# Optimization experiments

Measured on AMD Instinct MI355X. Metric: run time of the kernel, lower is better.

## Reference

```python
import jax, jax.numpy as jnp
import numpy as np

V, H, O = 32, 256, 256  # input_dim, hidden_dim, output_dim
EPS = 1e-5


def _layer_norm(x, g, b):
    m = jnp.mean(x, axis=-1, keepdims=True)
    v = jnp.mean((x - m) ** 2, axis=-1, keepdims=True)
    return g * (x - m) * jax.lax.rsqrt(v + EPS) + b


def setup_inputs() -> dict:
    key = jax.random.key(0)
    ks = jax.random.split(key, 20)
    s = 0.05
    inp = {
        "x": jax.random.normal(ks[0], (16, 256, V), dtype=jnp.float32),
        # selection GRN (input_dim -> input_dim, identity skip)
        "sel_fc1_w": jax.random.normal(ks[1], (V, H), dtype=jnp.float32) * s,
        "sel_fc1_b": jnp.zeros((H,), jnp.float32),
        "sel_fc2_w": jax.random.normal(ks[2], (H, V), dtype=jnp.float32) * s,
        "sel_fc2_b": jnp.zeros((V,), jnp.float32),
        "sel_gate_w": jax.random.normal(ks[3], (V, 2 * V), dtype=jnp.float32) * s,
        "sel_gate_b": jnp.zeros((2 * V,), jnp.float32),
        "sel_ln_g": jnp.ones((V,), jnp.float32),
        "sel_ln_b": jnp.zeros((V,), jnp.float32),
        # per-variable GRNs, stacked over the V variables (each has in_dim=1)
        "var_fc1_w": jax.random.normal(ks[4], (V, H), dtype=jnp.float32) * s,
        "var_fc1_b": jnp.zeros((V, H), jnp.float32),
        "var_fc2_w": jax.random.normal(ks[5], (V, H, O), dtype=jnp.float32) * s,
        "var_fc2_b": jnp.zeros((V, O), jnp.float32),
        "var_gate_w": jax.random.normal(ks[6], (V, 2 * O), dtype=jnp.float32) * s,
        "var_gate_b": jnp.zeros((V, 2 * O), jnp.float32),
        "var_skip_w": jax.random.normal(ks[7], (V, O), dtype=jnp.float32) * s,
        "var_skip_b": jnp.zeros((V, O), jnp.float32),
        "var_ln_g": jnp.ones((V, O), jnp.float32),
        "var_ln_b": jnp.zeros((V, O), jnp.float32),
    }
    return inp


def _vsn_forward(x, sel_fc1_w, sel_fc1_b, sel_fc2_w, sel_fc2_b, sel_gate_w,
                 sel_gate_b, sel_ln_g, sel_ln_b, var_fc1_w, var_fc1_b,
                 var_fc2_w, var_fc2_b, var_gate_w, var_gate_b, var_skip_w,
                 var_skip_b, var_ln_g, var_ln_b):
    B, S, _ = x.shape
    xr = x.reshape(-1, V)  # [N, V]

    # --- selection GRN (skip is identity) ---
    h = jax.nn.elu(xr @ sel_fc1_w + sel_fc1_b)        # [N, H]
    h = h @ sel_fc2_w + sel_fc2_b                      # [N, V] (unused by residual; matches torch code)
    g = xr @ sel_gate_w + sel_gate_b                   # [N, 2V]
    gates, values = jnp.split(g, 2, axis=-1)
    glu = jax.nn.sigmoid(gates) * values               # [N, V]
    sel = _layer_norm(glu + xr, sel_ln_g, sel_ln_b)    # [N, V]
    weights = jax.nn.softmax(sel, axis=-1)             # [N, V]

    # --- batched per-variable GRNs (in_dim = 1) ---
    xv = xr[..., None]                                  # [N, V, 1]
    hv = jax.nn.elu(xv * var_fc1_w + var_fc1_b)         # [N, V, H]
    hv = jnp.einsum('nvh,vho->nvo', hv, var_fc2_w) + var_fc2_b  # [N, V, O]
    gv = xv * var_gate_w + var_gate_b                   # [N, V, 2O]
    gates_v, values_v = jnp.split(gv, 2, axis=-1)
    glu_v = jax.nn.sigmoid(gates_v) * values_v          # [N, V, O]
    skip_v = xv * var_skip_w + var_skip_b               # [N, V, O]
    proc = _layer_norm(glu_v + skip_v, var_ln_g, var_ln_b)  # [N, V, O]

    out = jnp.einsum('nv,nvo->no', weights, proc)       # [N, O]
    return out.reshape(B, S, O)


def reference(x, sel_fc1_w, sel_fc1_b, sel_fc2_w, sel_fc2_b, sel_gate_w,
              sel_gate_b, sel_ln_g, sel_ln_b, var_fc1_w, var_fc1_b,
              var_fc2_w, var_fc2_b, var_gate_w, var_gate_b, var_skip_w,
              var_skip_b, var_ln_g, var_ln_b):
    return _vsn_forward(x, sel_fc1_w, sel_fc1_b, sel_fc2_w, sel_fc2_b,
                        sel_gate_w, sel_gate_b, sel_ln_g, sel_ln_b,
                        var_fc1_w, var_fc1_b, var_fc2_w, var_fc2_b,
                        var_gate_w, var_gate_b, var_skip_w, var_skip_b,
                        var_ln_g, var_ln_b)
```

## Files before the change

### kernel.cpp

```cpp
#include <hip/hip_runtime.h>
#include <hip/hip_bf16.h>


#define VDIM 32
#define ODIM 256
#define RPB  16
#define TPB  1024
#define NCHUNK  16

__device__ __forceinline__ float fast_sigmoid(float g) {
    return __builtin_amdgcn_rcpf(1.0f + __expf(-g));
}

template <int CTRL>
__device__ __forceinline__ float dpp_add(float x) {
    int s = __builtin_amdgcn_update_dpp(0, __builtin_bit_cast(int, x),
                                        CTRL, 0xF, 0xF, true);
    return x + __builtin_bit_cast(float, s);
}

__device__ __forceinline__ float wave_sum(float x) {
    x = dpp_add<0x111>(x);
    x = dpp_add<0x112>(x);
    x = dpp_add<0x114>(x);
    x = dpp_add<0x118>(x);
    x = dpp_add<0x142>(x);
    x = dpp_add<0x143>(x);
    return __builtin_bit_cast(float,
        __builtin_amdgcn_readlane(__builtin_bit_cast(int, x), 63));
}

__global__ void __launch_bounds__(TPB) vsn_fused(
    const float* __restrict__ x,
    const float* __restrict__ sgw,
    const float* __restrict__ sgb,
    const float* __restrict__ slg,
    const float* __restrict__ slb,
    const float* __restrict__ vgw,
    const float* __restrict__ vgb,
    const float* __restrict__ vsw,
    const float* __restrict__ vsb,
    const float* __restrict__ vlg,
    const float* __restrict__ vlb,
    float* __restrict__ out)
{
    __shared__ float wbuf[2][4096];
    __shared__ float x_s[RPB][VDIM];
    __shared__ float g_s[RPB][2 * VDIM];
    __shared__ float w_s[RPB][VDIM];

    const int tid  = threadIdx.x;
    const int row0 = blockIdx.x * RPB;

    const float* sbase;
    int sstr;
    if (tid < 256)      { sbase = vgw + (tid << 2);         sstr = 1024; }
    else if (tid < 512) { sbase = vgb + ((tid - 256) << 2); sstr = 1024; }
    else if (tid < 640) { sbase = vsw + ((tid - 512) << 2); sstr = 512;  }
    else if (tid < 768) { sbase = vsb + ((tid - 640) << 2); sstr = 512;  }
    else if (tid < 896) { sbase = vlg + ((tid - 768) << 2); sstr = 512;  }
    else                { sbase = vlb + ((tid - 896) << 2); sstr = 512;  }

    const float4 st0 = *(const float4*)sbase;

    if (tid < RPB * VDIM)
        ((float*)x_s)[tid] = x[row0 * VDIM + tid];
    __syncthreads();

    {
        const int r = tid >> 6, j = tid & 63;
        float acc = sgb[j];
        #pragma unroll
        for (int v = 0; v < VDIM; ++v)
            acc = fmaf(x_s[r][v], sgw[v * 64 + j], acc);
        g_s[r][j] = acc;
    }
    __syncthreads();

    ((float4*)wbuf[0])[tid] = st0;

    if (tid < RPB * VDIM) {
        const int r = tid >> 5, v = tid & 31;
        const float gate = g_s[r][v];
        const float val  = g_s[r][VDIM + v];
        const float y    = fast_sigmoid(gate) * val + x_s[r][v];
        float s1 = y, s2 = y * y;
        #pragma unroll
        for (int m = 1; m < 32; m <<= 1) {
            s1 += __shfl_xor(s1, m, 64);
            s2 += __shfl_xor(s2, m, 64);
        }
        const float mean = s1 * (1.0f / VDIM);
        const float var  = s2 * (1.0f / VDIM) - mean * mean;
        const float rs   = __builtin_amdgcn_rsqf(var + 1e-5f);
        const float sel  = slg[v] * ((y - mean) * rs) + slb[v];
        float mx = sel;
        #pragma unroll
        for (int m = 1; m < 32; m <<= 1)
            mx = fmaxf(mx, __shfl_xor(mx, m, 64));
        const float e = __expf(sel - mx);
        float se = e;
        #pragma unroll
        for (int m = 1; m < 32; m <<= 1)
            se += __shfl_xor(se, m, 64);
        w_s[r][v] = e * __builtin_amdgcn_rcpf(se);
    }
    __syncthreads();

    const int wave = tid >> 6;
    const int lane = tid & 63;
    const int o0   = lane << 2;

    float acc0 = 0.0f, acc1 = 0.0f, acc2 = 0.0f, acc3 = 0.0f;

    for (int c = 0; c < NCHUNK; ++c) {
        float4 pf;
        if (c < NCHUNK - 1)
            pf = *(const float4*)(sbase + (c + 1) * sstr);

        const float* buf = wbuf[c & 1];

        #pragma unroll
        for (int v4 = 0; v4 < 2; ++v4) {
            const int v = c * 2 + v4;
            const float4 ga  = *(const float4*)(buf + v4 * 512 + o0);
            const float4 va  = *(const float4*)(buf + v4 * 512 + 256 + o0);
            const float4 gab = *(const float4*)(buf + 1024 + v4 * 512 + o0);
            const float4 vab = *(const float4*)(buf + 1024 + v4 * 512 + 256 + o0);
            const float4 sw4 = *(const float4*)(buf + 2048 + v4 * 256 + o0);
            const float4 sb4 = *(const float4*)(buf + 2560 + v4 * 256 + o0);
            const float4 lg4 = *(const float4*)(buf + 3072 + v4 * 256 + o0);
            const float4 lb4 = *(const float4*)(buf + 3584 + v4 * 256 + o0);

            const float xv = x_s[wave][v];

            const float y0 = fast_sigmoid(fmaf(xv, ga.x, gab.x)) * fmaf(xv, va.x, vab.x) + fmaf(xv, sw4.x, sb4.x);
            const float y1 = fast_sigmoid(fmaf(xv, ga.y, gab.y)) * fmaf(xv, va.y, vab.y) + fmaf(xv, sw4.y, sb4.y);
            const float y2 = fast_sigmoid(fmaf(xv, ga.z, gab.z)) * fmaf(xv, va.z, vab.z) + fmaf(xv, sw4.z, sb4.z);
            const float y3 = fast_sigmoid(fmaf(xv, ga.w, gab.w)) * fmaf(xv, va.w, vab.w) + fmaf(xv, sw4.w, sb4.w);

            const float s1 = wave_sum((y0 + y1) + (y2 + y3));
            const float s2 = wave_sum(fmaf(y0, y0, fmaf(y1, y1, fmaf(y2, y2, y3 * y3))));

            const float mean = s1 * (1.0f / ODIM);
            const float var  = s2 * (1.0f / ODIM) - mean * mean;
            const float rs   = __builtin_amdgcn_rsqf(var + 1e-5f);
            const float wv   = w_s[wave][v];
            const float wrs  = wv * rs;
            acc0 = fmaf(lg4.x, (y0 - mean) * wrs, fmaf(wv, lb4.x, acc0));
            acc1 = fmaf(lg4.y, (y1 - mean) * wrs, fmaf(wv, lb4.y, acc1));
            acc2 = fmaf(lg4.z, (y2 - mean) * wrs, fmaf(wv, lb4.z, acc2));
            acc3 = fmaf(lg4.w, (y3 - mean) * wrs, fmaf(wv, lb4.w, acc3));
        }

        if (c < NCHUNK - 1)
            ((float4*)wbuf[(c + 1) & 1])[tid] = pf;
        __syncthreads();
    }

    float4 o4 = make_float4(acc0, acc1, acc2, acc3);
    *(float4*)(out + (size_t)(row0 + wave) * ODIM + o0) = o4;
}

extern "C" void kernel_launch(void* const* d_in, const int* in_sizes, int n_in,
                              void* d_out, int out_size, void* d_ws, size_t ws_size,
                              hipStream_t stream) {
    const float* x   = (const float*)d_in[0];
    const float* sgw = (const float*)d_in[5];
    const float* sgb = (const float*)d_in[6];
    const float* slg = (const float*)d_in[7];
    const float* slb = (const float*)d_in[8];
    const float* vgw = (const float*)d_in[13];
    const float* vgb = (const float*)d_in[14];
    const float* vsw = (const float*)d_in[15];
    const float* vsb = (const float*)d_in[16];
    const float* vlg = (const float*)d_in[17];
    const float* vlb = (const float*)d_in[18];
    float* out = (float*)d_out;

    const int N = in_sizes[0] / VDIM;
    const int grid = N / RPB;

    vsn_fused<<<grid, TPB, 0, stream>>>(x, sgw, sgb, slg, slb,
                                        vgw, vgb, vsw, vsb, vlg, vlb, out);
}
```

Before: 117.0 us.

## Keep per-variable weights in registers, reduce across waves with LDS atomics

Each wave now owns two variables and keeps their gate, value, skip and layernorm parameters in registers. It loops over all 16 rows of the block, where before each wave owned one row and streamed all the weights through a double-buffered LDS pipeline with a barrier per chunk. Per-row contributions are summed across waves with shared-memory atomicAdd, and the sigmoid folds the -log2(e) scale into the weights so it can use exp2. This removes the 16 barriers and the repeated weight traffic through LDS. In exchange it adds LDS atomic contention, higher register pressure, and a __launch_bounds__ occupancy hint.

```diff
diff --git a/kernel.cpp b/kernel.cpp
--- a/kernel.cpp
+++ b/kernel.cpp
@@ -6,11 +6,6 @@
 #define ODIM 256
 #define RPB  16
 #define TPB  1024
-#define NCHUNK  16
-
-__device__ __forceinline__ float fast_sigmoid(float g) {
-    return __builtin_amdgcn_rcpf(1.0f + __expf(-g));
-}
 
 template <int CTRL>
 __device__ __forceinline__ float dpp_add(float x) {
@@ -30,7 +25,11 @@
         __builtin_amdgcn_readlane(__builtin_bit_cast(int, x), 63));
 }
 
-__global__ void __launch_bounds__(TPB) vsn_fused(
+__device__ __forceinline__ float fast_sigmoid(float g) {
+    return __builtin_amdgcn_rcpf(1.0f + __expf(-g));
+}
+
+__global__ void __launch_bounds__(TPB, 4) vsn_fused(
     const float* __restrict__ x,
     const float* __restrict__ sgw,
     const float* __restrict__ sgb,
@@ -44,24 +43,37 @@
     const float* __restrict__ vlb,
     float* __restrict__ out)
 {
-    __shared__ float wbuf[2][4096];
+    __shared__ float acc_s[RPB * ODIM];
     __shared__ float x_s[RPB][VDIM];
     __shared__ float g_s[RPB][2 * VDIM];
     __shared__ float w_s[RPB][VDIM];
 
     const int tid  = threadIdx.x;
     const int row0 = blockIdx.x * RPB;
+    const int wave = tid >> 6;
+    const int lane = tid & 63;
+    const int v0   = wave * 2;
 
-    const float* sbase;
-    int sstr;
-    if (tid < 256)      { sbase = vgw + (tid << 2);         sstr = 1024; }
-    else if (tid < 512) { sbase = vgb + ((tid - 256) << 2); sstr = 1024; }
-    else if (tid < 640) { sbase = vsw + ((tid - 512) << 2); sstr = 512;  }
-    else if (tid < 768) { sbase = vsb + ((tid - 640) << 2); sstr = 512;  }
-    else if (tid < 896) { sbase = vlg + ((tid - 768) << 2); sstr = 512;  }
-    else                { sbase = vlb + ((tid - 896) << 2); sstr = 512;  }
+    float ga[2][4], gb[2][4], va[2][4], vb[2][4];
+    float sw[2][4], sb[2][4], lg[2][4], lb[2][4];
+    #pragma unroll
+    for (int j = 0; j < 2; ++j) {
+        const int v = v0 + j;
+        #pragma unroll
+        for (int k = 0; k < 4; ++k) {
+            const int c = lane + 64 * k;
+            ga[j][k] = vgw[v * 512 + c];
+            va[j][k] = vgw[v * 512 + 256 + c];
+            gb[j][k] = vgb[v * 512 + c];
+            vb[j][k] = vgb[v * 512 + 256 + c];
+            sw[j][k] = vsw[v * 256 + c];
+            sb[j][k] = vsb[v * 256 + c];
+            lg[j][k] = vlg[v * 256 + c];
+            lb[j][k] = vlb[v * 256 + c];
+        }
+    }
 
-    const float4 st0 = *(const float4*)sbase;
+    *(float4*)(acc_s + (tid << 2)) = make_float4(0.f, 0.f, 0.f, 0.f);
 
     if (tid < RPB * VDIM)
         ((float*)x_s)[tid] = x[row0 * VDIM + tid];
@@ -76,8 +88,6 @@
         g_s[r][j] = acc;
     }
     __syncthreads();
-
-    ((float4*)wbuf[0])[tid] = st0;
 
     if (tid < RPB * VDIM) {
         const int r = tid >> 5, v = tid & 31;
@@ -107,59 +117,57 @@
     }
     __syncthreads();
 
-    const int wave = tid >> 6;
-    const int lane = tid & 63;
-    const int o0   = lane << 2;
+    constexpr float NL2E = -1.4426950408889634f;
+    #pragma unroll
+    for (int j = 0; j < 2; ++j)
+        #pragma unroll
+        for (int k = 0; k < 4; ++k) { ga[j][k] *= NL2E; gb[j][k] *= NL2E; }
 
-    float acc0 = 0.0f, acc1 = 0.0f, acc2 = 0.0f, acc3 = 0.0f;
+    for (int i = 0; i < RPB; ++i) {
+        const int r  = (wave + i) & (RPB - 1);
+        const float xa = x_s[r][v0];
+        const float xb = x_s[r][v0 + 1];
+        const float wa = w_s[r][v0];
+        const float wb = w_s[r][v0 + 1];
 
-    for (int c = 0; c < NCHUNK; ++c) {
-        float4 pf;
-        if (c < NCHUNK - 1)
-            pf = *(const float4*)(sbase + (c + 1) * sstr);
+        float yA[4], yB[4];
+        #pragma unroll
+        for (int k = 0; k < 4; ++k) {
+            const float eA = __builtin_amdgcn_exp2f(fmaf(xa, ga[0][k], gb[0][k]));
+            const float sA = __builtin_amdgcn_rcpf(1.0f + eA);
+            yA[k] = fmaf(sA, fmaf(xa, va[0][k], vb[0][k]), fmaf(xa, sw[0][k], sb[0][k]));
+            const float eB = __builtin_amdgcn_exp2f(fmaf(xb, ga[1][k], gb[1][k]));
+            const float sB = __builtin_amdgcn_rcpf(1.0f + eB);
+            yB[k] = fmaf(sB, fmaf(xb, va[1][k], vb[1][k]), fmaf(xb, sw[1][k], sb[1][k]));
+        }
 
-        const float* buf = wbuf[c & 1];
+        const float s1a = wave_sum((yA[0] + yA[1]) + (yA[2] + yA[3]));
+        const float s2a = wave_sum(fmaf(yA[0], yA[0], fmaf(yA[1], yA[1],
+                                   fmaf(yA[2], yA[2], yA[3] * yA[3]))));
+        const float s1b = wave_sum((yB[0] + yB[1]) + (yB[2] + yB[3]));
+        const float s2b = wave_sum(fmaf(yB[0], yB[0], fmaf(yB[1], yB[1],
+                                   fmaf(yB[2], yB[2], yB[3] * yB[3]))));
+
+        const float mA  = s1a * (1.0f / ODIM);
+        const float vA  = s2a * (1.0f / ODIM) - mA * mA;
+        const float rsA = __builtin_amdgcn_rsqf(vA + 1e-5f);
+        const float wrsA = wa * rsA;
+        const float mB  = s1b * (1.0f / ODIM);
+        const float vB  = s2b * (1.0f / ODIM) - mB * mB;
+        const float rsB = __builtin_amdgcn_rsqf(vB + 1e-5f);
+        const float wrsB = wb * rsB;
 
         #pragma unroll
-        for (int v4 = 0; v4 < 2; ++v4) {
-            const int v = c * 2 + v4;
-            const float4 ga  = *(const float4*)(buf + v4 * 512 + o0);
-            const float4 va  = *(const float4*)(buf + v4 * 512 + 256 + o0);
-            const float4 gab = *(const float4*)(buf + 1024 + v4 * 512 + o0);
-            const float4 vab = *(const float4*)(buf + 1024 + v4 * 512 + 256 + o0);
-            const float4 sw4 = *(const float4*)(buf + 2048 + v4 * 256 + o0);
-            const float4 sb4 = *(const float4*)(buf + 2560 + v4 * 256 + o0);
-            const float4 lg4 = *(const float4*)(buf + 3072 + v4 * 256 + o0);
-            const float4 lb4 = *(const float4*)(buf + 3584 + v4 * 256 + o0);
+        for (int k = 0; k < 4; ++k) {
+            const float c = fmaf(lg[0][k], (yA[k] - mA) * wrsA, wa * lb[0][k])
+                          + fmaf(lg[1][k], (yB[k] - mB) * wrsB, wb * lb[1][k]);
+            atomicAdd(&acc_s[r * ODIM + lane + 64 * k], c);
+        }
+    }
+    __syncthreads();
 
-            const float xv = x_s[wave][v];
-
-            const float y0 = fast_sigmoid(fmaf(xv, ga.x, gab.x)) * fmaf(xv, va.x, vab.x) + fmaf(xv, sw4.x, sb4.x);
-            const float y1 = fast_sigmoid(fmaf(xv, ga.y, gab.y)) * fmaf(xv, va.y, vab.y) + fmaf(xv, sw4.y, sb4.y);
-            const float y2 = fast_sigmoid(fmaf(xv, ga.z, gab.z)) * fmaf(xv, va.z, vab.z) + fmaf(xv, sw4.z, sb4.z);
-            const float y3 = fast_sigmoid(fmaf(xv, ga.w, gab.w)) * fmaf(xv, va.w, vab.w) + fmaf(xv, sw4.w, sb4.w);
-
-            const float s1 = wave_sum((y0 + y1) + (y2 + y3));
-            const float s2 = wave_sum(fmaf(y0, y0, fmaf(y1, y1, fmaf(y2, y2, y3 * y3))));
-
-            const float mean = s1 * (1.0f / ODIM);
-            const float var  = s2 * (1.0f / ODIM) - mean * mean;
-            const float rs   = __builtin_amdgcn_rsqf(var + 1e-5f);
-            const float wv   = w_s[wave][v];
-            const float wrs  = wv * rs;
-            acc0 = fmaf(lg4.x, (y0 - mean) * wrs, fmaf(wv, lb4.x, acc0));
-            acc1 = fmaf(lg4.y, (y1 - mean) * wrs, fmaf(wv, lb4.y, acc1));
-            acc2 = fmaf(lg4.z, (y2 - mean) * wrs, fmaf(wv, lb4.z, acc2));
-            acc3 = fmaf(lg4.w, (y3 - mean) * wrs, fmaf(wv, lb4.w, acc3));
-        }
-
-        if (c < NCHUNK - 1)
-            ((float4*)wbuf[(c + 1) & 1])[tid] = pf;
-        __syncthreads();
-    }
-
-    float4 o4 = make_float4(acc0, acc1, acc2, acc3);
-    *(float4*)(out + (size_t)(row0 + wave) * ODIM + o0) = o4;
+    const float4 o4 = *(const float4*)(acc_s + wave * ODIM + (lane << 2));
+    *(float4*)(out + (size_t)(row0 + wave) * ODIM + (lane << 2)) = o4;
 }
 
 extern "C" void kernel_launch(void* const* d_in, const int* in_sizes, int n_in,
```

New measurement: 195.4 us. 66.9% more time.
